# Performance work log

Hardware: AMD Instinct MI355X
Metric: run time of the kernel (lower is better)

## Reference

```python
import jax, jax.numpy as jnp
import numpy as np

N_HEADS = 4
N_HIDDEN = 64  # out_features // n_heads
NEG_SLOPE = 0.2


def setup_inputs() -> dict:
    key = jax.random.key(0)
    k1, k2, k3, k4, k5 = jax.random.split(key, 5)
    B, N, F_IN, F_OUT = 1, 4096, 128, 256
    h = jax.random.normal(k1, (B, N, F_IN), dtype=jnp.float32)
    adj_mat = jax.random.uniform(k2, (N, N, 1), dtype=jnp.float32)
    W_proj = jax.random.normal(k3, (F_IN, N_HEADS * N_HIDDEN), dtype=jnp.float32) / np.sqrt(F_IN)
    W_proj_attn = jax.random.normal(k4, (F_IN, N_HEADS * N_HIDDEN // 2), dtype=jnp.float32) / np.sqrt(F_IN)
    w_attn = jax.random.normal(k5, (N_HIDDEN,), dtype=jnp.float32) / np.sqrt(N_HIDDEN)
    return {"h": h, "adj_mat": adj_mat, "W_proj": W_proj, "W_proj_attn": W_proj_attn, "w_attn": w_attn}


def reference(h, adj_mat, W_proj, W_proj_attn, w_attn):
    B, N, _ = h.shape
    H, D = N_HEADS, N_HIDDEN
    half = D // 2
    # value projection: (B, N, H, D)
    g = (h @ W_proj).reshape(B, N, H, D)
    # attention-feature projection: (B, N, H, D//2)
    ga = (h @ W_proj_attn).reshape(B, N, H, half)
    # attn(cat([ga_i, ga_j])) decomposes linearly: e_ij = <w_l, ga_i> + <w_r, ga_j>
    # (identical math to the torch repeat/cat/Linear, without the NxNxD tensor)
    el = jnp.einsum('bnhk,k->bnh', ga, w_attn[:half])   # dest node i term
    er = jnp.einsum('bnhk,k->bnh', ga, w_attn[half:])   # source node j term
    e = jax.nn.leaky_relu(el[:, :, None, :] + er[:, None, :, :], NEG_SLOPE)  # (B, N, N, H)
    mask = adj_mat >= 0.5  # (N, N, 1) broadcasts over (B, N, N, H)
    e = jnp.where(mask, e, -jnp.inf)
    a = jax.nn.softmax(e, axis=2)  # softmax over source nodes j
    # dropout is identity in eval mode
    out = jnp.einsum('bijh,bjhf->bihf', a, g)  # (B, N, H, D)
    return out.reshape(B, N, H * D)  # is_concat=True
```

## Files before the change

### kernel.cpp

```cpp
#include <hip/hip_runtime.h>
#include <hip/hip_bf16.h>

typedef __bf16 bf16_t;
typedef __bf16 bf16x4 __attribute__((ext_vector_type(4)));
typedef __bf16 bf16x8 __attribute__((ext_vector_type(8)));
typedef float floatx4 __attribute__((ext_vector_type(4)));
typedef unsigned int u32;

#define N_NODES 4096
#define F_IN 128
#define NUM_HEADS 4
#define D_HID 64
#define F_OUT 256
#define NEG_SLOPE 0.2f
#define LOG2E 1.4426950408889634f
#define NWORDS 128

__global__ __launch_bounds__(256) void mask_kernel(
    const float* __restrict__ adj, u32* __restrict__ maskw)
{
    const int w = blockIdx.x * 256 + threadIdx.x;
    const float* src = adj + (size_t)w * 32;
    u32 bits = 0;
#pragma unroll
    for (int c = 0; c < 8; ++c) {
        const float4 v = *reinterpret_cast<const float4*>(src + c * 4);
        bits |= (u32)(v.x >= 0.5f) << (4 * c + 0);
        bits |= (u32)(v.y >= 0.5f) << (4 * c + 1);
        bits |= (u32)(v.z >= 0.5f) << (4 * c + 2);
        bits |= (u32)(v.w >= 0.5f) << (4 * c + 3);
    }
    maskw[w] = bits;
}

__global__ __launch_bounds__(384) void proj_kernel(
    const float* __restrict__ hmat, const float* __restrict__ Wp,
    const float* __restrict__ Wa, const float* __restrict__ wattn,
    bf16_t* __restrict__ GB, float* __restrict__ el, float* __restrict__ er)
{
    const int t = threadIdx.x;
    const int j0 = blockIdx.x * 4;

    float acc[4] = {0.f, 0.f, 0.f, 0.f};

    const float* wptr;
    int stride;
    if (t < 256) { wptr = Wp + t;         stride = 256; }
    else         { wptr = Wa + (t - 256); stride = 128; }

    const float* hbase = hmat + (size_t)j0 * F_IN;

    for (int m = 0; m < F_IN; m += 4) {
        const float w0 = wptr[(size_t)(m + 0) * stride];
        const float w1 = wptr[(size_t)(m + 1) * stride];
        const float w2 = wptr[(size_t)(m + 2) * stride];
        const float w3 = wptr[(size_t)(m + 3) * stride];
#pragma unroll
        for (int jl = 0; jl < 4; ++jl) {
            const float4 hv = *reinterpret_cast<const float4*>(&hbase[jl * F_IN + m]);
            acc[jl] = fmaf(hv.w, w3, fmaf(hv.z, w2, fmaf(hv.y, w1, fmaf(hv.x, w0, acc[jl]))));
        }
    }

    if (t < 256) {
        const int h = t >> 6, f = t & 63;
        bf16x4 o;
#pragma unroll
        for (int q = 0; q < 4; ++q) o[q] = (bf16_t)acc[q];
        const size_t base = ((((size_t)h * 128 + (j0 >> 5)) * 4 + (f >> 4)) * 64
                             + (f & 15) + 16 * ((j0 >> 3) & 3)) * 8 + (j0 & 7);
        *reinterpret_cast<bf16x4*>(&GB[base]) = o;
    } else {
        const int ta = t - 256;
        const int ha = ta >> 5, k = ta & 31;
        const float wl = wattn[k] * LOG2E, wr = wattn[32 + k] * LOG2E;
#pragma unroll
        for (int jl = 0; jl < 4; ++jl) {
            float vl = acc[jl] * wl;
            float vr = acc[jl] * wr;
#pragma unroll
            for (int s = 16; s >= 1; s >>= 1) {
                vl += __shfl_xor(vl, s, 64);
                vr += __shfl_xor(vr, s, 64);
            }
            if (k == 0) {
                el[ha * N_NODES + j0 + jl] = vl;
                er[ha * N_NODES + j0 + jl] = vr;
            }
        }
    }
}

__global__ __launch_bounds__(256, 4) void attn_kernel(
    const u32* __restrict__ maskw, const bf16_t* __restrict__ GB,
    const float* __restrict__ el, const float* __restrict__ er,
    float* __restrict__ numout, float* __restrict__ den_g,
    int ntiles)
{
    const int tid  = threadIdx.x;
    const int i0   = blockIdx.x * 32;
    const int jc   = blockIdx.y;
    const int hh   = tid >> 6;
    const int lane = tid & 63;
    const int m    = lane & 15;
    const int quad = lane >> 4;
    const int NS   = ntiles * 2;
    const int j32_0 = (jc * ntiles * 64) >> 5;

    const float el_lo = el[hh * N_NODES + i0 + m];
    const float el_hi = el[hh * N_NODES + i0 + 16 + m];
    const u32* mrowL = maskw + (size_t)(i0 + m) * NWORDS;
    const u32* mrowH = mrowL + (size_t)16 * NWORDS;
    const float* erp = er + hh * N_NODES + quad * 8;
    const bf16_t* gb = GB + (size_t)hh * (128 * 4 * 512) + lane * 8;

    floatx4 accL0 = {0.f, 0.f, 0.f, 0.f};
    floatx4 accL1 = accL0, accL2 = accL0, accL3 = accL0, accdL = accL0;
    floatx4 accH0 = accL0, accH1 = accL0, accH2 = accL0, accH3 = accL0, accdH = accL0;
    bf16x8 ones;
#pragma unroll
    for (int q = 0; q < 8; ++q) ones[q] = (bf16_t)1.0f;

    u32 mLc = mrowL[j32_0], mHc = mrowH[j32_0];
    float4 e0c = *reinterpret_cast<const float4*>(erp + j32_0 * 32);
    float4 e1c = *reinterpret_cast<const float4*>(erp + j32_0 * 32 + 4);
    const bf16_t* gp0 = gb + (size_t)j32_0 * 2048;
    bf16x8 b0c = *reinterpret_cast<const bf16x8*>(gp0);
    bf16x8 b1c = *reinterpret_cast<const bf16x8*>(gp0 + 512);
    bf16x8 b2c = *reinterpret_cast<const bf16x8*>(gp0 + 1024);
    bf16x8 b3c = *reinterpret_cast<const bf16x8*>(gp0 + 1536);

    for (int s = 0; s < NS; ++s) {
        u32 mLn = 0, mHn = 0;
        float4 e0n = {0.f, 0.f, 0.f, 0.f}, e1n = e0n;
        bf16x8 b0n = {}, b1n = {}, b2n = {}, b3n = {};
        if (s + 1 < NS) {
            const int jn = j32_0 + s + 1;
            mLn = mrowL[jn];
            mHn = mrowH[jn];
            e0n = *reinterpret_cast<const float4*>(erp + jn * 32);
            e1n = *reinterpret_cast<const float4*>(erp + jn * 32 + 4);
            const bf16_t* gp = gb + (size_t)jn * 2048;
            b0n = *reinterpret_cast<const bf16x8*>(gp);
            b1n = *reinterpret_cast<const bf16x8*>(gp + 512);
            b2n = *reinterpret_cast<const bf16x8*>(gp + 1024);
            b3n = *reinterpret_cast<const bf16x8*>(gp + 1536);
        }
        const u32 byL = (mLc >> (quad * 8)) & 0xff;
        const u32 byH = (mHc >> (quad * 8)) & 0xff;
        const float ev[8] = {e0c.x, e0c.y, e0c.z, e0c.w, e1c.x, e1c.y, e1c.z, e1c.w};
        bf16x8 afL, afH;
#pragma unroll
        for (int q = 0; q < 8; ++q) {
            const float sL = el_lo + ev[q];
            const float sH = el_hi + ev[q];
            const float pL = __builtin_amdgcn_exp2f(fmaxf(sL, NEG_SLOPE * sL));
            const float pH = __builtin_amdgcn_exp2f(fmaxf(sH, NEG_SLOPE * sH));
            afL[q] = (bf16_t)(((byL >> q) & 1u) ? pL : 0.0f);
            afH[q] = (bf16_t)(((byH >> q) & 1u) ? pH : 0.0f);
        }
        accdL = __builtin_amdgcn_mfma_f32_16x16x32_bf16(afL, ones, accdL, 0, 0, 0);
        accdH = __builtin_amdgcn_mfma_f32_16x16x32_bf16(afH, ones, accdH, 0, 0, 0);
        accL0 = __builtin_amdgcn_mfma_f32_16x16x32_bf16(afL, b0c, accL0, 0, 0, 0);
        accH0 = __builtin_amdgcn_mfma_f32_16x16x32_bf16(afH, b0c, accH0, 0, 0, 0);
        accL1 = __builtin_amdgcn_mfma_f32_16x16x32_bf16(afL, b1c, accL1, 0, 0, 0);
        accH1 = __builtin_amdgcn_mfma_f32_16x16x32_bf16(afH, b1c, accH1, 0, 0, 0);
        accL2 = __builtin_amdgcn_mfma_f32_16x16x32_bf16(afL, b2c, accL2, 0, 0, 0);
        accH2 = __builtin_amdgcn_mfma_f32_16x16x32_bf16(afH, b2c, accH2, 0, 0, 0);
        accL3 = __builtin_amdgcn_mfma_f32_16x16x32_bf16(afL, b3c, accL3, 0, 0, 0);
        accH3 = __builtin_amdgcn_mfma_f32_16x16x32_bf16(afH, b3c, accH3, 0, 0, 0);
        mLc = mLn; mHc = mHn; e0c = e0n; e1c = e1n;
        b0c = b0n; b1c = b1n; b2c = b2n; b3c = b3n;
    }

    float* nrow = numout + (size_t)jc * ((size_t)N_NODES * F_OUT);
    const int ibL = i0 + quad * 4;
    const int ibH = ibL + 16;
#pragma unroll
    for (int r = 0; r < 4; ++r) {
        float* dL = nrow + (size_t)(ibL + r) * F_OUT + hh * D_HID + m;
        dL[0]  = accL0[r];
        dL[16] = accL1[r];
        dL[32] = accL2[r];
        dL[48] = accL3[r];
        float* dH = nrow + (size_t)(ibH + r) * F_OUT + hh * D_HID + m;
        dH[0]  = accH0[r];
        dH[16] = accH1[r];
        dH[32] = accH2[r];
        dH[48] = accH3[r];
    }
    if (m == 0) {
#pragma unroll
        for (int r = 0; r < 4; ++r) {
            den_g[((size_t)jc * N_NODES + ibL + r) * NUM_HEADS + hh] = accdL[r];
            den_g[((size_t)jc * N_NODES + ibH + r) * NUM_HEADS + hh] = accdH[r];
        }
    }
}

template<int NJC>
__global__ __launch_bounds__(256) void reduce_kernel(
    const float* __restrict__ num, const float* __restrict__ den,
    float* __restrict__ out)
{
    const int t4   = blockIdx.x * 256 + threadIdx.x;
    const int base = t4 * 4;
    const int i  = base >> 8;
    const int hh = (base & 255) >> 6;
    float4 n = {0.f, 0.f, 0.f, 0.f};
    float d = 0.f;
#pragma unroll
    for (int jc = 0; jc < NJC; ++jc) {
        const float4 v = *reinterpret_cast<const float4*>(
            num + (size_t)jc * ((size_t)N_NODES * F_OUT) + base);
        n.x += v.x; n.y += v.y; n.z += v.z; n.w += v.w;
        d += den[((size_t)jc * N_NODES + i) * NUM_HEADS + hh];
    }
    const float rd = 1.0f / d;
    float4 o = {n.x * rd, n.y * rd, n.z * rd, n.w * rd};
    *reinterpret_cast<float4*>(out + base) = o;
}

extern "C" void kernel_launch(void* const* d_in, const int* in_sizes, int n_in,
                              void* d_out, int out_size, void* d_ws, size_t ws_size,
                              hipStream_t stream)
{
    const float* hmat = (const float*)d_in[0];
    const float* adj  = (const float*)d_in[1];
    const float* Wp   = (const float*)d_in[2];
    const float* Wa   = (const float*)d_in[3];
    const float* watt = (const float*)d_in[4];
    float* out = (float*)d_out;

    char* ws = (char*)d_ws;
    bf16_t* GB   = (bf16_t*)ws;
    float*  el   = (float*)(ws + (2ull << 20));
    float*  er   = (float*)(ws + (2ull << 20) + (64ull << 10));
    u32*    mskw = (u32*)(ws + (2ull << 20) + (128ull << 10));
    const size_t baseoff = (4ull << 20) + (128ull << 10);

    const size_t num_bytes = (size_t)N_NODES * F_OUT * 4;
    const size_t den_bytes = (size_t)N_NODES * NUM_HEADS * 4;
    const int njc = (ws_size >= baseoff + 8 * (num_bytes + den_bytes)) ? 8
                  : (ws_size >= baseoff + 4 * (num_bytes + den_bytes)) ? 4 : 2;

    float* num = (float*)(ws + baseoff);
    float* den = (float*)(ws + baseoff + (size_t)njc * num_bytes);

    proj_kernel<<<1024, 384, 0, stream>>>(hmat, Wp, Wa, watt, GB, el, er);
    mask_kernel<<<(N_NODES * NWORDS) / 256, 256, 0, stream>>>(adj, mskw);
    attn_kernel<<<dim3(128, njc), 256, 0, stream>>>(mskw, GB, el, er, num, den,
                                                    (N_NODES / njc) / 64);
    if (njc == 8)      reduce_kernel<8><<<(N_NODES * F_OUT) / 1024, 256, 0, stream>>>(num, den, out);
    else if (njc == 4) reduce_kernel<4><<<(N_NODES * F_OUT) / 1024, 256, 0, stream>>>(num, den, out);
    else               reduce_kernel<2><<<(N_NODES * F_OUT) / 1024, 256, 0, stream>>>(num, den, out);
}
```

Before: 159.9 us.

## Halve attention row tile, compute denominator on VALU, drop manual prefetch

The attention kernel now handles 16 destination rows per block instead of 32 and launches twice as many blocks with a higher occupancy hint. The softmax denominator MFMA against a ones vector is replaced by a scalar running sum plus cross-lane shuffles, and exp2 is skipped for masked entries. The explicit register double-buffering of next-iteration loads is removed to cut register pressure. In exchange each block rereads the value and er tiles for half as many rows, doubling global/L2 traffic for GB, and the loads are no longer prefetched a step ahead.

```diff
diff --git a/kernel.cpp b/kernel.cpp
--- a/kernel.cpp
+++ b/kernel.cpp
@@ -91,111 +91,95 @@
     }
 }
 
-__global__ __launch_bounds__(256, 4) void attn_kernel(
+__global__ __launch_bounds__(256, 8) void attn_kernel(
     const u32* __restrict__ maskw, const bf16_t* __restrict__ GB,
     const float* __restrict__ el, const float* __restrict__ er,
     float* __restrict__ numout, float* __restrict__ den_g,
     int ntiles)
 {
     const int tid  = threadIdx.x;
-    const int i0   = blockIdx.x * 32;
+    const int i0   = blockIdx.x * 16;
     const int jc   = blockIdx.y;
     const int hh   = tid >> 6;
     const int lane = tid & 63;
     const int m    = lane & 15;
     const int quad = lane >> 4;
     const int NS   = ntiles * 2;
-    const int j32_0 = (jc * ntiles * 64) >> 5;
-
-    const float el_lo = el[hh * N_NODES + i0 + m];
-    const float el_hi = el[hh * N_NODES + i0 + 16 + m];
-    const u32* mrowL = maskw + (size_t)(i0 + m) * NWORDS;
-    const u32* mrowH = mrowL + (size_t)16 * NWORDS;
-    const float* erp = er + hh * N_NODES + quad * 8;
-    const bf16_t* gb = GB + (size_t)hh * (128 * 4 * 512) + lane * 8;
-
-    floatx4 accL0 = {0.f, 0.f, 0.f, 0.f};
-    floatx4 accL1 = accL0, accL2 = accL0, accL3 = accL0, accdL = accL0;
-    floatx4 accH0 = accL0, accH1 = accL0, accH2 = accL0, accH3 = accL0, accdH = accL0;
-    bf16x8 ones;
-#pragma unroll
-    for (int q = 0; q < 8; ++q) ones[q] = (bf16_t)1.0f;
-
-    u32 mLc = mrowL[j32_0], mHc = mrowH[j32_0];
-    float4 e0c = *reinterpret_cast<const float4*>(erp + j32_0 * 32);
-    float4 e1c = *reinterpret_cast<const float4*>(erp + j32_0 * 32 + 4);
-    const bf16_t* gp0 = gb + (size_t)j32_0 * 2048;
-    bf16x8 b0c = *reinterpret_cast<const bf16x8*>(gp0);
-    bf16x8 b1c = *reinterpret_cast<const bf16x8*>(gp0 + 512);
-    bf16x8 b2c = *reinterpret_cast<const bf16x8*>(gp0 + 1024);
-    bf16x8 b3c = *reinterpret_cast<const bf16x8*>(gp0 + 1536);
-
+    const int j32_0 = jc * NS;
+
+    const float el_i = el[hh * N_NODES + i0 + m];
+    const u32*  mrow = maskw + (size_t)(i0 + m) * NWORDS + j32_0;
+    const float* erp = er + hh * N_NODES + j32_0 * 32 + quad * 8;
+    const bf16_t* gb = GB + (size_t)hh * (128 * 4 * 512)
+                          + (size_t)j32_0 * 2048 + lane * 8;
+
+    floatx4 acc0 = {0.f, 0.f, 0.f, 0.f};
+    floatx4 acc1 = acc0, acc2 = acc0, acc3 = acc0;
+    float den = 0.f;
+
+    u32 mc = mrow[0];
     for (int s = 0; s < NS; ++s) {
-        u32 mLn = 0, mHn = 0;
-        float4 e0n = {0.f, 0.f, 0.f, 0.f}, e1n = e0n;
-        bf16x8 b0n = {}, b1n = {}, b2n = {}, b3n = {};
-        if (s + 1 < NS) {
-            const int jn = j32_0 + s + 1;
-            mLn = mrowL[jn];
-            mHn = mrowH[jn];
-            e0n = *reinterpret_cast<const float4*>(erp + jn * 32);
-            e1n = *reinterpret_cast<const float4*>(erp + jn * 32 + 4);
-            const bf16_t* gp = gb + (size_t)jn * 2048;
-            b0n = *reinterpret_cast<const bf16x8*>(gp);
-            b1n = *reinterpret_cast<const bf16x8*>(gp + 512);
-            b2n = *reinterpret_cast<const bf16x8*>(gp + 1024);
-            b3n = *reinterpret_cast<const bf16x8*>(gp + 1536);
-        }
-        const u32 byL = (mLc >> (quad * 8)) & 0xff;
-        const u32 byH = (mHc >> (quad * 8)) & 0xff;
-        const float ev[8] = {e0c.x, e0c.y, e0c.z, e0c.w, e1c.x, e1c.y, e1c.z, e1c.w};
-        bf16x8 afL, afH;
-#pragma unroll
-        for (int q = 0; q < 8; ++q) {
-            const float sL = el_lo + ev[q];
-            const float sH = el_hi + ev[q];
-            const float pL = __builtin_amdgcn_exp2f(fmaxf(sL, NEG_SLOPE * sL));
-            const float pH = __builtin_amdgcn_exp2f(fmaxf(sH, NEG_SLOPE * sH));
-            afL[q] = (bf16_t)(((byL >> q) & 1u) ? pL : 0.0f);
-            afH[q] = (bf16_t)(((byH >> q) & 1u) ? pH : 0.0f);
-        }
-        accdL = __builtin_amdgcn_mfma_f32_16x16x32_bf16(afL, ones, accdL, 0, 0, 0);
-        accdH = __builtin_amdgcn_mfma_f32_16x16x32_bf16(afH, ones, accdH, 0, 0, 0);
-        accL0 = __builtin_amdgcn_mfma_f32_16x16x32_bf16(afL, b0c, accL0, 0, 0, 0);
-        accH0 = __builtin_amdgcn_mfma_f32_16x16x32_bf16(afH, b0c, accH0, 0, 0, 0);
-        accL1 = __builtin_amdgcn_mfma_f32_16x16x32_bf16(afL, b1c, accL1, 0, 0, 0);
-        accH1 = __builtin_amdgcn_mfma_f32_16x16x32_bf16(afH, b1c, accH1, 0, 0, 0);
-        accL2 = __builtin_amdgcn_mfma_f32_16x16x32_bf16(afL, b2c, accL2, 0, 0, 0);
-        accH2 = __builtin_amdgcn_mfma_f32_16x16x32_bf16(afH, b2c, accH2, 0, 0, 0);
-        accL3 = __builtin_amdgcn_mfma_f32_16x16x32_bf16(afL, b3c, accL3, 0, 0, 0);
-        accH3 = __builtin_amdgcn_mfma_f32_16x16x32_bf16(afH, b3c, accH3, 0, 0, 0);
-        mLc = mLn; mHc = mHn; e0c = e0n; e1c = e1n;
-        b0c = b0n; b1c = b1n; b2c = b2n; b3c = b3n;
-    }
+        const u32 mn = mrow[(s + 1 < NS) ? s + 1 : s];
+        const float4 e0 = *reinterpret_cast<const float4*>(erp);
+        const float4 e1 = *reinterpret_cast<const float4*>(erp + 4);
+        const bf16x8 b0 = *reinterpret_cast<const bf16x8*>(gb);
+        const bf16x8 b1 = *reinterpret_cast<const bf16x8*>(gb + 512);
+        const bf16x8 b2 = *reinterpret_cast<const bf16x8*>(gb + 1024);
+        const bf16x8 b3 = *reinterpret_cast<const bf16x8*>(gb + 1536);
+
+        const u32 by = (mc >> (quad * 8)) & 0xffu;
+
+        float s0 = el_i + e0.x; s0 = fmaxf(s0, NEG_SLOPE * s0);
+        float s1 = el_i + e0.y; s1 = fmaxf(s1, NEG_SLOPE * s1);
+        float s2 = el_i + e0.z; s2 = fmaxf(s2, NEG_SLOPE * s2);
+        float s3 = el_i + e0.w; s3 = fmaxf(s3, NEG_SLOPE * s3);
+        float s4 = el_i + e1.x; s4 = fmaxf(s4, NEG_SLOPE * s4);
+        float s5 = el_i + e1.y; s5 = fmaxf(s5, NEG_SLOPE * s5);
+        float s6 = el_i + e1.z; s6 = fmaxf(s6, NEG_SLOPE * s6);
+        float s7 = el_i + e1.w; s7 = fmaxf(s7, NEG_SLOPE * s7);
+
+        const float p0 = (by &   1u) ? __builtin_amdgcn_exp2f(s0) : 0.f;
+        const float p1 = (by &   2u) ? __builtin_amdgcn_exp2f(s1) : 0.f;
+        const float p2 = (by &   4u) ? __builtin_amdgcn_exp2f(s2) : 0.f;
+        const float p3 = (by &   8u) ? __builtin_amdgcn_exp2f(s3) : 0.f;
+        const float p4 = (by &  16u) ? __builtin_amdgcn_exp2f(s4) : 0.f;
+        const float p5 = (by &  32u) ? __builtin_amdgcn_exp2f(s5) : 0.f;
+        const float p6 = (by &  64u) ? __builtin_amdgcn_exp2f(s6) : 0.f;
+        const float p7 = (by & 128u) ? __builtin_amdgcn_exp2f(s7) : 0.f;
+
+        den += ((p0 + p1) + (p2 + p3)) + ((p4 + p5) + (p6 + p7));
+
+        bf16x8 af;
+        af[0] = (bf16_t)p0; af[1] = (bf16_t)p1;
+        af[2] = (bf16_t)p2; af[3] = (bf16_t)p3;
+        af[4] = (bf16_t)p4; af[5] = (bf16_t)p5;
+        af[6] = (bf16_t)p6; af[7] = (bf16_t)p7;
+
+        acc0 = __builtin_amdgcn_mfma_f32_16x16x32_bf16(af, b0, acc0, 0, 0, 0);
+        acc1 = __builtin_amdgcn_mfma_f32_16x16x32_bf16(af, b1, acc1, 0, 0, 0);
+        acc2 = __builtin_amdgcn_mfma_f32_16x16x32_bf16(af, b2, acc2, 0, 0, 0);
+        acc3 = __builtin_amdgcn_mfma_f32_16x16x32_bf16(af, b3, acc3, 0, 0, 0);
+
+        mc = mn;
+        erp += 32;
+        gb  += 2048;
+    }
+
+    den += __shfl_xor(den, 16, 64);
+    den += __shfl_xor(den, 32, 64);
 
     float* nrow = numout + (size_t)jc * ((size_t)N_NODES * F_OUT);
-    const int ibL = i0 + quad * 4;
-    const int ibH = ibL + 16;
+    const int ib = i0 + quad * 4;
 #pragma unroll
     for (int r = 0; r < 4; ++r) {
-        float* dL = nrow + (size_t)(ibL + r) * F_OUT + hh * D_HID + m;
-        dL[0]  = accL0[r];
-        dL[16] = accL1[r];
-        dL[32] = accL2[r];
-        dL[48] = accL3[r];
-        float* dH = nrow + (size_t)(ibH + r) * F_OUT + hh * D_HID + m;
-        dH[0]  = accH0[r];
-        dH[16] = accH1[r];
-        dH[32] = accH2[r];
-        dH[48] = accH3[r];
-    }
-    if (m == 0) {
-#pragma unroll
-        for (int r = 0; r < 4; ++r) {
-            den_g[((size_t)jc * N_NODES + ibL + r) * NUM_HEADS + hh] = accdL[r];
-            den_g[((size_t)jc * N_NODES + ibH + r) * NUM_HEADS + hh] = accdH[r];
-        }
-    }
+        float* dst = nrow + (size_t)(ib + r) * F_OUT + hh * D_HID + m;
+        dst[0]  = acc0[r];
+        dst[16] = acc1[r];
+        dst[32] = acc2[r];
+        dst[48] = acc3[r];
+    }
+    if (quad == 0)
+        den_g[((size_t)jc * N_NODES + i0 + m) * NUM_HEADS + hh] = den;
 }
 
 template<int NJC>
@@ -249,7 +233,7 @@
 
     proj_kernel<<<1024, 384, 0, stream>>>(hmat, Wp, Wa, watt, GB, el, er);
     mask_kernel<<<(N_NODES * NWORDS) / 256, 256, 0, stream>>>(adj, mskw);
-    attn_kernel<<<dim3(128, njc), 256, 0, stream>>>(mskw, GB, el, er, num, den,
+    attn_kernel<<<dim3(256, njc), 256, 0, stream>>>(mskw, GB, el, er, num, den,
                                                     (N_NODES / njc) / 64);
     if (njc == 8)      reduce_kernel<8><<<(N_NODES * F_OUT) / 1024, 256, 0, stream>>>(num, den, out);
     else if (njc == 4) reduce_kernel<4><<<(N_NODES * F_OUT) / 1024, 256, 0, stream>>>(num, den, out);
```

Measured after the change: 168.2 us. 1.05x slower.

## Remap attention blocks to one head per block, compute denominators on VALU

Applied to the files above, without the earlier changes.

The attention kernel now assigns each block a single head (grid z), with its four waves covering 128 destination rows, so the waves share the same G and er tiles instead of each wave handling a different head. The softmax denominator is accumulated with scalar adds plus a shuffle reduction instead of two extra MFMAs against a ones vector, and exp2 is evaluated only for unmasked entries. The prefetch is made branchless by clamping the next-tile offset, with the pointers advanced each step. The projection kernel handles 8 nodes per block so each thread writes a full bf16x8 vector.

```diff
diff --git a/kernel.cpp b/kernel.cpp
--- a/kernel.cpp
+++ b/kernel.cpp
@@ -39,9 +39,9 @@
     bf16_t* __restrict__ GB, float* __restrict__ el, float* __restrict__ er)
 {
     const int t = threadIdx.x;
-    const int j0 = blockIdx.x * 4;
-
-    float acc[4] = {0.f, 0.f, 0.f, 0.f};
+    const int j0 = blockIdx.x * 8;
+
+    float acc[8] = {0.f, 0.f, 0.f, 0.f, 0.f, 0.f, 0.f, 0.f};
 
     const float* wptr;
     int stride;
@@ -56,7 +56,7 @@
         const float w2 = wptr[(size_t)(m + 2) * stride];
         const float w3 = wptr[(size_t)(m + 3) * stride];
 #pragma unroll
-        for (int jl = 0; jl < 4; ++jl) {
+        for (int jl = 0; jl < 8; ++jl) {
             const float4 hv = *reinterpret_cast<const float4*>(&hbase[jl * F_IN + m]);
             acc[jl] = fmaf(hv.w, w3, fmaf(hv.z, w2, fmaf(hv.y, w1, fmaf(hv.x, w0, acc[jl]))));
         }
@@ -64,18 +64,18 @@
 
     if (t < 256) {
         const int h = t >> 6, f = t & 63;
-        bf16x4 o;
-#pragma unroll
-        for (int q = 0; q < 4; ++q) o[q] = (bf16_t)acc[q];
+        bf16x8 o;
+#pragma unroll
+        for (int q = 0; q < 8; ++q) o[q] = (bf16_t)acc[q];
         const size_t base = ((((size_t)h * 128 + (j0 >> 5)) * 4 + (f >> 4)) * 64
-                             + (f & 15) + 16 * ((j0 >> 3) & 3)) * 8 + (j0 & 7);
-        *reinterpret_cast<bf16x4*>(&GB[base]) = o;
+                             + (f & 15) + 16 * ((j0 >> 3) & 3)) * 8;
+        *reinterpret_cast<bf16x8*>(&GB[base]) = o;
     } else {
         const int ta = t - 256;
         const int ha = ta >> 5, k = ta & 31;
         const float wl = wattn[k] * LOG2E, wr = wattn[32 + k] * LOG2E;
 #pragma unroll
-        for (int jl = 0; jl < 4; ++jl) {
+        for (int jl = 0; jl < 8; ++jl) {
             float vl = acc[jl] * wl;
             float vr = acc[jl] * wr;
 #pragma unroll
@@ -98,69 +98,67 @@
     int ntiles)
 {
     const int tid  = threadIdx.x;
-    const int i0   = blockIdx.x * 32;
+    const int wave = tid >> 6;
+    const int i0   = blockIdx.x * 128 + wave * 32;
     const int jc   = blockIdx.y;
-    const int hh   = tid >> 6;
+    const int hh   = blockIdx.z;
     const int lane = tid & 63;
     const int m    = lane & 15;
     const int quad = lane >> 4;
     const int NS   = ntiles * 2;
-    const int j32_0 = (jc * ntiles * 64) >> 5;
+    const int j32_0 = jc * NS;
 
     const float el_lo = el[hh * N_NODES + i0 + m];
     const float el_hi = el[hh * N_NODES + i0 + 16 + m];
-    const u32* mrowL = maskw + (size_t)(i0 + m) * NWORDS;
-    const u32* mrowH = mrowL + (size_t)16 * NWORDS;
-    const float* erp = er + hh * N_NODES + quad * 8;
-    const bf16_t* gb = GB + (size_t)hh * (128 * 4 * 512) + lane * 8;
+    const u32*  mrowL = maskw + (size_t)(i0 + m) * NWORDS + j32_0;
+    const u32*  mrowH = mrowL + (size_t)16 * NWORDS;
+    const float* erp  = er + hh * N_NODES + j32_0 * 32 + quad * 8;
+    const bf16_t* gb  = GB + (size_t)hh * (128 * 4 * 512)
+                           + (size_t)j32_0 * 2048 + lane * 8;
 
     floatx4 accL0 = {0.f, 0.f, 0.f, 0.f};
-    floatx4 accL1 = accL0, accL2 = accL0, accL3 = accL0, accdL = accL0;
-    floatx4 accH0 = accL0, accH1 = accL0, accH2 = accL0, accH3 = accL0, accdH = accL0;
-    bf16x8 ones;
-#pragma unroll
-    for (int q = 0; q < 8; ++q) ones[q] = (bf16_t)1.0f;
-
-    u32 mLc = mrowL[j32_0], mHc = mrowH[j32_0];
-    float4 e0c = *reinterpret_cast<const float4*>(erp + j32_0 * 32);
-    float4 e1c = *reinterpret_cast<const float4*>(erp + j32_0 * 32 + 4);
-    const bf16_t* gp0 = gb + (size_t)j32_0 * 2048;
-    bf16x8 b0c = *reinterpret_cast<const bf16x8*>(gp0);
-    bf16x8 b1c = *reinterpret_cast<const bf16x8*>(gp0 + 512);
-    bf16x8 b2c = *reinterpret_cast<const bf16x8*>(gp0 + 1024);
-    bf16x8 b3c = *reinterpret_cast<const bf16x8*>(gp0 + 1536);
+    floatx4 accL1 = accL0, accL2 = accL0, accL3 = accL0;
+    floatx4 accH0 = accL0, accH1 = accL0, accH2 = accL0, accH3 = accL0;
+    float denL = 0.f, denH = 0.f;
+
+    u32 mLc = mrowL[0], mHc = mrowH[0];
+    float4 e0c = *reinterpret_cast<const float4*>(erp);
+    float4 e1c = *reinterpret_cast<const float4*>(erp + 4);
+    bf16x8 b0c = *reinterpret_cast<const bf16x8*>(gb);
+    bf16x8 b1c = *reinterpret_cast<const bf16x8*>(gb + 512);
+    bf16x8 b2c = *reinterpret_cast<const bf16x8*>(gb + 1024);
+    bf16x8 b3c = *reinterpret_cast<const bf16x8*>(gb + 1536);
 
     for (int s = 0; s < NS; ++s) {
-        u32 mLn = 0, mHn = 0;
-        float4 e0n = {0.f, 0.f, 0.f, 0.f}, e1n = e0n;
-        bf16x8 b0n = {}, b1n = {}, b2n = {}, b3n = {};
-        if (s + 1 < NS) {
-            const int jn = j32_0 + s + 1;
-            mLn = mrowL[jn];
-            mHn = mrowH[jn];
-            e0n = *reinterpret_cast<const float4*>(erp + jn * 32);
-            e1n = *reinterpret_cast<const float4*>(erp + jn * 32 + 4);
-            const bf16_t* gp = gb + (size_t)jn * 2048;
-            b0n = *reinterpret_cast<const bf16x8*>(gp);
-            b1n = *reinterpret_cast<const bf16x8*>(gp + 512);
-            b2n = *reinterpret_cast<const bf16x8*>(gp + 1024);
-            b3n = *reinterpret_cast<const bf16x8*>(gp + 1536);
+        const int d = (s + 1 < NS) ? 1 : 0;
+        const u32    mLn = mrowL[d];
+        const u32    mHn = mrowH[d];
+        const float4 e0n = *reinterpret_cast<const float4*>(erp + d * 32);
+        const float4 e1n = *reinterpret_cast<const float4*>(erp + d * 32 + 4);
+        const bf16_t* gpn = gb + (size_t)d * 2048;
+        const bf16x8 b0n = *reinterpret_cast<const bf16x8*>(gpn);
+        const bf16x8 b1n = *reinterpret_cast<const bf16x8*>(gpn + 512);
+        const bf16x8 b2n = *reinterpret_cast<const bf16x8*>(gpn + 1024);
+        const bf16x8 b3n = *reinterpret_cast<const bf16x8*>(gpn + 1536);
+
+        const u32 byL = (mLc >> (quad * 8)) & 0xffu;
+        const u32 byH = (mHc >> (quad * 8)) & 0xffu;
+        const float ev[8] = {e0c.x, e0c.y, e0c.z, e0c.w, e1c.x, e1c.y, e1c.z, e1c.w};
+
+        bf16x8 afL, afH;
+        float dL = 0.f, dH = 0.f;
+#pragma unroll
+        for (int q = 0; q < 8; ++q) {
+            float sL = el_lo + ev[q]; sL = fmaxf(sL, NEG_SLOPE * sL);
+            float sH = el_hi + ev[q]; sH = fmaxf(sH, NEG_SLOPE * sH);
+            const float pL = ((byL >> q) & 1u) ? __builtin_amdgcn_exp2f(sL) : 0.f;
+            const float pH = ((byH >> q) & 1u) ? __builtin_amdgcn_exp2f(sH) : 0.f;
+            dL += pL; dH += pH;
+            afL[q] = (bf16_t)pL;
+            afH[q] = (bf16_t)pH;
         }
-        const u32 byL = (mLc >> (quad * 8)) & 0xff;
-        const u32 byH = (mHc >> (quad * 8)) & 0xff;
-        const float ev[8] = {e0c.x, e0c.y, e0c.z, e0c.w, e1c.x, e1c.y, e1c.z, e1c.w};
-        bf16x8 afL, afH;
-#pragma unroll
-        for (int q = 0; q < 8; ++q) {
-            const float sL = el_lo + ev[q];
-            const float sH = el_hi + ev[q];
-            const float pL = __builtin_amdgcn_exp2f(fmaxf(sL, NEG_SLOPE * sL));
-            const float pH = __builtin_amdgcn_exp2f(fmaxf(sH, NEG_SLOPE * sH));
-            afL[q] = (bf16_t)(((byL >> q) & 1u) ? pL : 0.0f);
-            afH[q] = (bf16_t)(((byH >> q) & 1u) ? pH : 0.0f);
-        }
-        accdL = __builtin_amdgcn_mfma_f32_16x16x32_bf16(afL, ones, accdL, 0, 0, 0);
-        accdH = __builtin_amdgcn_mfma_f32_16x16x32_bf16(afH, ones, accdH, 0, 0, 0);
+        denL += dL; denH += dH;
+
         accL0 = __builtin_amdgcn_mfma_f32_16x16x32_bf16(afL, b0c, accL0, 0, 0, 0);
         accH0 = __builtin_amdgcn_mfma_f32_16x16x32_bf16(afH, b0c, accH0, 0, 0, 0);
         accL1 = __builtin_amdgcn_mfma_f32_16x16x32_bf16(afL, b1c, accL1, 0, 0, 0);
@@ -169,9 +167,18 @@
         accH2 = __builtin_amdgcn_mfma_f32_16x16x32_bf16(afH, b2c, accH2, 0, 0, 0);
         accL3 = __builtin_amdgcn_mfma_f32_16x16x32_bf16(afL, b3c, accL3, 0, 0, 0);
         accH3 = __builtin_amdgcn_mfma_f32_16x16x32_bf16(afH, b3c, accH3, 0, 0, 0);
+
         mLc = mLn; mHc = mHn; e0c = e0n; e1c = e1n;
         b0c = b0n; b1c = b1n; b2c = b2n; b3c = b3n;
-    }
+        mrowL += 1; mrowH += 1;
+        erp += 32;
+        gb  += 2048;
+    }
+
+    denL += __shfl_xor(denL, 16, 64);
+    denL += __shfl_xor(denL, 32, 64);
+    denH += __shfl_xor(denH, 16, 64);
+    denH += __shfl_xor(denH, 32, 64);
 
     float* nrow = numout + (size_t)jc * ((size_t)N_NODES * F_OUT);
     const int ibL = i0 + quad * 4;
@@ -189,12 +196,9 @@
         dH[32] = accH2[r];
         dH[48] = accH3[r];
     }
-    if (m == 0) {
-#pragma unroll
-        for (int r = 0; r < 4; ++r) {
-            den_g[((size_t)jc * N_NODES + ibL + r) * NUM_HEADS + hh] = accdL[r];
-            den_g[((size_t)jc * N_NODES + ibH + r) * NUM_HEADS + hh] = accdH[r];
-        }
+    if (quad == 0) {
+        den_g[((size_t)jc * N_NODES + i0 + m) * NUM_HEADS + hh] = denL;
+        den_g[((size_t)jc * N_NODES + i0 + 16 + m) * NUM_HEADS + hh] = denH;
     }
 }
 
@@ -247,10 +251,10 @@
     float* num = (float*)(ws + baseoff);
     float* den = (float*)(ws + baseoff + (size_t)njc * num_bytes);
 
-    proj_kernel<<<1024, 384, 0, stream>>>(hmat, Wp, Wa, watt, GB, el, er);
+    proj_kernel<<<512, 384, 0, stream>>>(hmat, Wp, Wa, watt, GB, el, er);
     mask_kernel<<<(N_NODES * NWORDS) / 256, 256, 0, stream>>>(adj, mskw);
-    attn_kernel<<<dim3(128, njc), 256, 0, stream>>>(mskw, GB, el, er, num, den,
-                                                    (N_NODES / njc) / 64);
+    attn_kernel<<<dim3(32, njc, NUM_HEADS), 256, 0, stream>>>(
+        mskw, GB, el, er, num, den, (N_NODES / njc) / 64);
     if (njc == 8)      reduce_kernel<8><<<(N_NODES * F_OUT) / 1024, 256, 0, stream>>>(num, den, out);
     else if (njc == 4) reduce_kernel<4><<<(N_NODES * F_OUT) / 1024, 256, 0, stream>>>(num, den, out);
     else               reduce_kernel<2><<<(N_NODES * F_OUT) / 1024, 256, 0, stream>>>(num, den, out);
```

New measurement: 165.9 us. 1.04x slower.
